# Kernel optimization log

Hardware: AMD Instinct MI355X
Metric: run time of the kernel (lower is better)

Reference implementation:

```python
import jax, jax.numpy as jnp
import numpy as np

E = 1024   # embedding_size
H = 16     # num_heads
DH = E // H


def setup_inputs() -> dict:
    key = jax.random.key(0)
    ks = jax.random.split(key, 11)
    B, S = 2, 2048
    std = 0.02
    return {
        "query": jax.random.normal(ks[0], (B, S, E), jnp.float32),
        "key": jax.random.normal(ks[1], (B, S, E), jnp.float32),
        "value": jax.random.normal(ks[2], (B, S, E), jnp.float32),
        "Wq": jax.random.normal(ks[3], (E, E), jnp.float32) * std,
        "bq": jnp.zeros((E,), jnp.float32),
        "Wk": jax.random.normal(ks[4], (E, E), jnp.float32) * std,
        "bk": jnp.zeros((E,), jnp.float32),
        "Wv": jax.random.normal(ks[5], (E, E), jnp.float32) * std,
        "bv": jnp.zeros((E,), jnp.float32),
        "Wo": jax.random.normal(ks[6], (E, E), jnp.float32) * std,
        "bo": jnp.zeros((E,), jnp.float32),
    }


def _split_heads(x, B, S):
    # [B,S,E] -> [B,H,S,DH]
    return x.reshape(B, S, H, DH).transpose(0, 2, 1, 3)


def reference(query, key, value, Wq, bq, Wk, bk, Wv, bv, Wo, bo):
    B, S, _ = query.shape
    # torch Linear: y = x @ W.T + b
    q = _split_heads(query @ Wq.T + bq, B, S)
    k = _split_heads(key @ Wk.T + bk, B, key.shape[1])
    v = _split_heads(value @ Wv.T + bv, B, value.shape[1])
    # naive unscaled attention (original has no 1/sqrt(d) factor)
    scores = jnp.einsum("bhsd,bhtd->bhst", q, k)  # [B,H,S,T]
    attn = jax.nn.softmax(scores, axis=-1)
    out = jnp.einsum("bhst,bhtd->bhsd", attn, v)  # [B,H,S,DH]
    out = out.transpose(0, 2, 1, 3).reshape(B, S, E)
    return out @ Wo.T + bo
```

## Files before the change

### kernel.cpp

```cpp
#include <hip/hip_runtime.h>
#include <hip/hip_bf16.h>

constexpr int kB   = 2;
constexpr int kS   = 2048;
constexpr int kE   = 1024;
constexpr int kH   = 16;
constexpr int kDH  = 64;
constexpr int kTok = kB * kS;

typedef short bf16x8 __attribute__((ext_vector_type(8)));
typedef float f32x4  __attribute__((ext_vector_type(4)));
typedef unsigned int uint2v __attribute__((ext_vector_type(2)));

__device__ __forceinline__ float bf2f(unsigned short s) {
  union { unsigned int u; float f; } c; c.u = ((unsigned int)s) << 16; return c.f;
}
__device__ __forceinline__ unsigned short f2bf(float f) {
  union { float f; unsigned int u; } c; c.f = f;
  unsigned int u = c.u;
  u += 0x7fffu + ((u >> 16) & 1u);
  return (unsigned short)(u >> 16);
}

__device__ __forceinline__ unsigned cvtpk(float lo, float hi) {
  unsigned r;
  asm("v_cvt_pk_bf16_f32 %0, %1, %2" : "=v"(r) : "v"(lo), "v"(hi));
  return r;
}

__device__ __forceinline__ void gl_lds16(const unsigned short* g, unsigned short* l) {
  __builtin_amdgcn_global_load_lds(
      (const __attribute__((address_space(1))) unsigned int*)g,
      (__attribute__((address_space(3))) unsigned int*)l, 16, 0, 0);
}

__global__ void detect_dtype(const unsigned short* __restrict__ q, int* flag) {
  __shared__ int cnt;
  if (threadIdx.x == 0) cnt = 0;
  __syncthreads();
  int bad = 0;
  for (int i = threadIdx.x; i < 4096; i += 256) {
    unsigned int e = (q[i] >> 7) & 0xFF;
    if (e >= 0xC0) bad++;
  }
  atomicAdd(&cnt, bad);
  __syncthreads();
  if (threadIdx.x == 0) *flag = (cnt > 8) ? 1 : 0;
}

struct Seg { const void* src; unsigned short* dst; unsigned int n; unsigned int blk0; };
struct ConvArgs { Seg s[11]; };

__global__ __launch_bounds__(256) void conv_all(ConvArgs a, const int* __restrict__ flag) {
  const unsigned int bid = blockIdx.x;
  int si = 0;
  #pragma unroll
  for (int i = 1; i < 11; ++i)
    if (bid >= a.s[i].blk0) si = i;
  const Seg sg = a.s[si];
  const int i0 = ((int)(bid - sg.blk0) * 256 + threadIdx.x) * 8;
  if (i0 >= (int)sg.n) return;
  if (*flag) {
    const float* s = (const float*)sg.src + i0;
    f32x4 f0 = *(const f32x4*)(s);
    f32x4 f1 = *(const f32x4*)(s + 4);
    bf16x8 v;
    #pragma unroll
    for (int j = 0; j < 4; ++j) v[j]     = (short)f2bf(f0[j]);
    #pragma unroll
    for (int j = 0; j < 4; ++j) v[j + 4] = (short)f2bf(f1[j]);
    *(bf16x8*)&sg.dst[i0] = v;
  } else {
    *(bf16x8*)&sg.dst[i0] = *(const bf16x8*)((const unsigned short*)sg.src + i0);
  }
}

__device__ __forceinline__ void gemm_core(
    const unsigned short* __restrict__ A,
    const unsigned short* __restrict__ W,
    int Kdim, int bM, int bN,
    unsigned short* As, unsigned short* Ws,
    f32x4 acc[4][4])
{
  const int tid  = threadIdx.x;
  const int lane = tid & 63;
  const int wv   = tid >> 6;
  const int wm   = (wv >> 1) * 64;
  const int wn   = (wv & 1) * 64;
  const int lr   = lane & 15;
  const int kq   = (lane >> 4) * 8;

  const int r0 = tid >> 2;
  const int c0 = (tid & 3) * 8;

  const unsigned short* Ag = A + (size_t)(bM + r0) * Kdim + c0;
  const unsigned short* Wg = W + (size_t)(bN + r0) * Kdim + c0;
  unsigned short* lA = &As[tid * 8];
  unsigned short* lW = &Ws[tid * 8];

  for (int k0 = 0; k0 < Kdim; k0 += 32) {
    gl_lds16(Ag + k0,                      lA);
    gl_lds16(Ag + (size_t)64 * Kdim + k0,  lA + 2048);
    gl_lds16(Wg + k0,                      lW);
    gl_lds16(Wg + (size_t)64 * Kdim + k0,  lW + 2048);
    __syncthreads();

    bf16x8 a[4], b[4];
    #pragma unroll
    for (int i = 0; i < 4; ++i)
      a[i] = *(const bf16x8*)&As[(wm + i * 16 + lr) * 32 + kq];
    #pragma unroll
    for (int i = 0; i < 4; ++i)
      b[i] = *(const bf16x8*)&Ws[(wn + i * 16 + lr) * 32 + kq];
    #pragma unroll
    for (int i = 0; i < 4; ++i)
      #pragma unroll
      for (int j = 0; j < 4; ++j)
        acc[i][j] = __builtin_amdgcn_mfma_f32_16x16x32_bf16(a[i], b[j], acc[i][j], 0, 0, 0);
    __syncthreads();
  }
}

__global__ __launch_bounds__(256) void gemm_qkv(
    const unsigned short* __restrict__ Abase,
    const unsigned short* __restrict__ Wbase,
    const unsigned short* __restrict__ biasbase,
    unsigned short* __restrict__ Cbase)
{
  __shared__ unsigned short As[128 * 32];
  __shared__ unsigned short Ws[128 * 32];

  const int z = blockIdx.z;
  const unsigned short* A    = Abase    + (size_t)z * (kTok * kE);
  const unsigned short* W    = Wbase    + (size_t)z * (kE * kE);
  const unsigned short* bias = biasbase + (size_t)z * kE;
  unsigned short* C          = Cbase    + (size_t)z * (kTok * kE);

  const int bM = blockIdx.y * 128;
  const int bN = blockIdx.x * 128;

  f32x4 acc[4][4] = {};
  gemm_core(A, W, kE, bM, bN, As, Ws, acc);

  const int lane = threadIdx.x & 63;
  const int wv   = threadIdx.x >> 6;
  const int wm   = (wv >> 1) * 64;
  const int wn   = (wv & 1) * 64;
  const int lr   = lane & 15;
  const int qd   = lane >> 4;
  #pragma unroll
  for (int j = 0; j < 4; ++j) {
    const int col = bN + wn + j * 16 + lr;
    const float bb = bf2f(bias[col]);
    #pragma unroll
    for (int i = 0; i < 4; ++i)
      #pragma unroll
      for (int r = 0; r < 4; ++r) {
        const int row = bM + wm + i * 16 + qd * 4 + r;
        C[(size_t)row * kE + col] = f2bf(acc[i][j][r] + bb);
      }
  }
}

__global__ __launch_bounds__(256) void vtrans(
    const unsigned short* __restrict__ Vb,
    unsigned short* __restrict__ Vt)
{
  __shared__ unsigned short Lt[64 * 72];
  const int tid = threadIdx.x;
  const int bh  = blockIdx.y;
  const int b   = bh >> 4;
  const int h   = bh & 15;
  const int hcol = h * kDH;
  const int s0  = blockIdx.x * 64;

  #pragma unroll
  for (int issue = 0; issue < 2; ++issue) {
    int g = issue * 256 + tid;
    int r = g >> 3, c = (g & 7) * 8;
    bf16x8 vv = *(const bf16x8*)&Vb[(size_t)(b * kS + s0 + r) * kE + hcol + c];
    const int swz = ((((r >> 3) ^ (c >> 3)) & 7) << 3) + (r & 7);
    #pragma unroll
    for (int i = 0; i < 8; ++i)
      Lt[(c + i) * 72 + swz] = (unsigned short)vv[i];
  }
  __syncthreads();
  #pragma unroll
  for (int issue = 0; issue < 2; ++issue) {
    int g = issue * 256 + tid;
    int f = g >> 3, tc = (g & 7) * 8;
    const int blk = ((tc >> 3) ^ (f >> 3)) & 7;
    bf16x8 vv = *(const bf16x8*)&Lt[f * 72 + (blk << 3)];
    *(bf16x8*)&Vt[(size_t)b * (kE * kS) + (size_t)(hcol + f) * kS + s0 + tc] = vv;
  }
}

__global__ __launch_bounds__(256) void gemm_out(
    const unsigned short* __restrict__ A,
    const unsigned short* __restrict__ W,
    const unsigned short* __restrict__ bias,
    void* __restrict__ C,
    const int* __restrict__ flag)
{
  __shared__ unsigned short As[128 * 32];
  __shared__ unsigned short Ws[128 * 32];

  const int bM = blockIdx.y * 128;
  const int bN = blockIdx.x * 128;

  f32x4 acc[4][4] = {};
  gemm_core(A, W, kE, bM, bN, As, Ws, acc);

  const int lane = threadIdx.x & 63;
  const int wv   = threadIdx.x >> 6;
  const int wm   = (wv >> 1) * 64;
  const int wn   = (wv & 1) * 64;
  const int lr   = lane & 15;
  const int qd   = lane >> 4;
  if (*flag) {
    float* Cf = (float*)C;
    #pragma unroll
    for (int j = 0; j < 4; ++j) {
      const int col = bN + wn + j * 16 + lr;
      const float bb = bf2f(bias[col]);
      #pragma unroll
      for (int i = 0; i < 4; ++i)
        #pragma unroll
        for (int r = 0; r < 4; ++r) {
          const int row = bM + wm + i * 16 + qd * 4 + r;
          Cf[(size_t)row * kE + col] = acc[i][j][r] + bb;
        }
    }
  } else {
    unsigned short* Cb = (unsigned short*)C;
    #pragma unroll
    for (int j = 0; j < 4; ++j) {
      const int col = bN + wn + j * 16 + lr;
      const float bb = bf2f(bias[col]);
      #pragma unroll
      for (int i = 0; i < 4; ++i)
        #pragma unroll
        for (int r = 0; r < 4; ++r) {
          const int row = bM + wm + i * 16 + qd * 4 + r;
          Cb[(size_t)row * kE + col] = f2bf(acc[i][j][r] + bb);
        }
    }
  }
}

__global__ __launch_bounds__(256) void attn(
    const unsigned short* __restrict__ Qb,
    const unsigned short* __restrict__ Kb,
    const unsigned short* __restrict__ Vt,
    unsigned short* __restrict__ Ob)
{
  __shared__ unsigned short Ks[64 * 72];
  __shared__ unsigned short Vs[64 * 72];

  const int tid  = threadIdx.x;
  const int lane = tid & 63;
  const int w    = tid >> 6;
  const int lr   = lane & 15;
  const int quad = lane >> 4;
  const int kq   = quad * 8;

  const int bh = blockIdx.y;
  const int b  = bh >> 4;
  const int h  = bh & 15;
  const int q0 = blockIdx.x * 128;

  const size_t rowbase = (size_t)b * kS * kE;
  const int hcol = h * kDH;
  const unsigned short* Vbase = Vt + (size_t)b * (kE * kS) + (size_t)hcol * kS;

  const int r0 = tid >> 3;
  const int c0 = (tid & 7) * 8;

  bf16x8 aq[2][2];
  #pragma unroll
  for (int rg = 0; rg < 2; ++rg)
    #pragma unroll
    for (int hh = 0; hh < 2; ++hh)
      aq[rg][hh] = *(const bf16x8*)
          &Qb[rowbase + (size_t)(q0 + w * 32 + rg * 16 + lr) * kE + hcol + hh * 32 + kq];

  f32x4 o[2][4] = {};
  float l4[2][4] = {};

  bf16x8 rk0 = *(const bf16x8*)&Kb[rowbase + (size_t)(r0)      * kE + hcol + c0];
  bf16x8 rk1 = *(const bf16x8*)&Kb[rowbase + (size_t)(r0 + 32) * kE + hcol + c0];
  bf16x8 rv0 = *(const bf16x8*)&Vbase[(size_t)(r0)      * kS + c0];
  bf16x8 rv1 = *(const bf16x8*)&Vbase[(size_t)(r0 + 32) * kS + c0];

  for (int t0 = 0; t0 < kS; t0 += 64) {
    __syncthreads();
    *(bf16x8*)&Ks[ r0       * 72 + c0] = rk0;
    *(bf16x8*)&Ks[(r0 + 32) * 72 + c0] = rk1;
    *(bf16x8*)&Vs[ r0       * 72 + c0] = rv0;
    *(bf16x8*)&Vs[(r0 + 32) * 72 + c0] = rv1;
    __syncthreads();

    const int t1 = t0 + 64;
    if (t1 < kS) {
      rk0 = *(const bf16x8*)&Kb[rowbase + (size_t)(t1 + r0)      * kE + hcol + c0];
      rk1 = *(const bf16x8*)&Kb[rowbase + (size_t)(t1 + r0 + 32) * kE + hcol + c0];
      rv0 = *(const bf16x8*)&Vbase[(size_t)(r0)      * kS + t1 + c0];
      rv1 = *(const bf16x8*)&Vbase[(size_t)(r0 + 32) * kS + t1 + c0];
    }

    f32x4 s[2][4];
    #pragma unroll
    for (int rg = 0; rg < 2; ++rg)
      #pragma unroll
      for (int tn = 0; tn < 4; ++tn)
        s[rg][tn] = f32x4{0.f, 0.f, 0.f, 0.f};
    #pragma unroll
    for (int tn = 0; tn < 4; ++tn) {
      const bf16x8 bk0 = *(const bf16x8*)&Ks[(tn * 16 + lr) * 72 + 0 + kq];
      const bf16x8 bk1 = *(const bf16x8*)&Ks[(tn * 16 + lr) * 72 + 32 + kq];
      #pragma unroll
      for (int rg = 0; rg < 2; ++rg) {
        s[rg][tn] = __builtin_amdgcn_mfma_f32_16x16x32_bf16(bk0, aq[rg][0], s[rg][tn], 0, 0, 0);
        s[rg][tn] = __builtin_amdgcn_mfma_f32_16x16x32_bf16(bk1, aq[rg][1], s[rg][tn], 0, 0, 0);
      }
    }

    #pragma unroll
    for (int rg = 0; rg < 2; ++rg)
      #pragma unroll
      for (int tn = 0; tn < 4; ++tn)
        #pragma unroll
        for (int r = 0; r < 4; ++r) {
          const float e = __expf(s[rg][tn][r]);
          s[rg][tn][r] = e;
          l4[rg][r] += e;
        }

    bf16x8 ap[2][2];
    #pragma unroll
    for (int rg = 0; rg < 2; ++rg)
      #pragma unroll
      for (int kk = 0; kk < 2; ++kk) {
        const unsigned A0 = cvtpk(s[rg][2 * kk][0],     s[rg][2 * kk][1]);
        const unsigned A1 = cvtpk(s[rg][2 * kk + 1][0], s[rg][2 * kk + 1][1]);
        const uint2v u   = __builtin_amdgcn_permlane32_swap(A0, A1, false, false);
        const uint2v z02 = __builtin_amdgcn_permlane16_swap(u[0], u[1], false, false);
        const unsigned B0 = cvtpk(s[rg][2 * kk][2],     s[rg][2 * kk][3]);
        const unsigned B1 = cvtpk(s[rg][2 * kk + 1][2], s[rg][2 * kk + 1][3]);
        const uint2v v2  = __builtin_amdgcn_permlane32_swap(B0, B1, false, false);
        const uint2v z13 = __builtin_amdgcn_permlane16_swap(v2[0], v2[1], false, false);
        union { unsigned ud[4]; bf16x8 v; } pk;
        pk.ud[0] = z02[0];
        pk.ud[1] = z13[0];
        pk.ud[2] = z02[1];
        pk.ud[3] = z13[1];
        ap[rg][kk] = pk.v;
      }

    #pragma unroll
    for (int kk = 0; kk < 2; ++kk)
      #pragma unroll
      for (int dt = 0; dt < 4; ++dt) {
        const bf16x8 bv = *(const bf16x8*)&Vs[(dt * 16 + lr) * 72 + kk * 32 + kq];
        #pragma unroll
        for (int rg = 0; rg < 2; ++rg)
          o[rg][dt] = __builtin_amdgcn_mfma_f32_16x16x32_bf16(ap[rg][kk], bv, o[rg][dt], 0, 0, 0);
      }
  }

  #pragma unroll
  for (int rg = 0; rg < 2; ++rg) {
    float l = (l4[rg][0] + l4[rg][1]) + (l4[rg][2] + l4[rg][3]);
    l += __shfl_xor(l, 16, 64);
    l += __shfl_xor(l, 32, 64);
    float inv[4];
    #pragma unroll
    for (int r = 0; r < 4; ++r)
      inv[r] = 1.0f / __shfl(l, quad * 4 + r, 64);

    #pragma unroll
    for (int dt = 0; dt < 4; ++dt) {
      #pragma unroll
      for (int r = 0; r < 4; ++r) {
        const int row = q0 + w * 32 + rg * 16 + quad * 4 + r;
        const int col = hcol + dt * 16 + lr;
        Ob[rowbase + (size_t)row * kE + col] = f2bf(o[rg][dt][r] * inv[r]);
      }
    }
  }
}

extern "C" void kernel_launch(void* const* d_in, const int* in_sizes, int n_in,
                              void* d_out, int out_size, void* d_ws, size_t ws_size,
                              hipStream_t stream) {
  const int nQKV = kTok * kE;
  const int nW   = kE * kE;
  const int nB   = kE;

  char* wsb = (char*)d_ws;
  int* flag = (int*)wsb;
  unsigned short* qc  = (unsigned short*)(wsb + 16);
  unsigned short* kc  = qc  + (size_t)nQKV;
  unsigned short* vc  = kc  + (size_t)nQKV;
  unsigned short* Wqc = vc  + (size_t)nQKV;
  unsigned short* Wkc = Wqc + (size_t)nW;
  unsigned short* Wvc = Wkc + (size_t)nW;
  unsigned short* Woc = Wvc + (size_t)nW;
  unsigned short* bqc = Woc + (size_t)nW;
  unsigned short* bkc = bqc + nB;
  unsigned short* bvc = bkc + nB;
  unsigned short* boc = bvc + nB;
  unsigned short* Qb  = boc + nB;
  unsigned short* Kb  = Qb  + (size_t)nQKV;
  unsigned short* Vb  = Kb  + (size_t)nQKV;
  unsigned short* Vtb = kc;
  unsigned short* Ob  = qc;

  detect_dtype<<<1, 256, 0, stream>>>((const unsigned short*)d_in[0], flag);

  ConvArgs ca;
  const void* srcs[11] = { d_in[0], d_in[1], d_in[2], d_in[3], d_in[4], d_in[5],
                           d_in[6], d_in[7], d_in[8], d_in[9], d_in[10] };
  unsigned short* dsts[11] = { qc, kc, vc, Wqc, bqc, Wkc, bkc, Wvc, bvc, Woc, boc };
  const unsigned int ns[11] = { (unsigned)nQKV, (unsigned)nQKV, (unsigned)nQKV,
                                (unsigned)nW, (unsigned)nB, (unsigned)nW, (unsigned)nB,
                                (unsigned)nW, (unsigned)nB, (unsigned)nW, (unsigned)nB };
  unsigned int blk = 0;
  for (int i = 0; i < 11; ++i) {
    ca.s[i].src = srcs[i]; ca.s[i].dst = dsts[i]; ca.s[i].n = ns[i]; ca.s[i].blk0 = blk;
    blk += (ns[i] + 2047) / 2048;
  }
  conv_all<<<blk, 256, 0, stream>>>(ca, flag);

  dim3 blk256(256);
  dim3 gqkv(kE / 128, kTok / 128, 3);
  gemm_qkv<<<gqkv, blk256, 0, stream>>>(qc, Wqc, bqc, Qb);

  dim3 gvt(kS / 64, kB * kH);
  vtrans<<<gvt, blk256, 0, stream>>>(Vb, Vtb);

  dim3 gattn(kS / 128, kB * kH);
  attn<<<gattn, blk256, 0, stream>>>(Qb, Kb, Vtb, Ob);

  dim3 gout(kE / 128, kTok / 128);
  gemm_out<<<gout, blk256, 0, stream>>>(Ob, Woc, boc, d_out, flag);
}
```

Baseline: 267.6 us.

## Double-buffer K/V tiles in attention and fold log2e into Wq for exp2

```diff
diff --git a/kernel.cpp b/kernel.cpp
--- a/kernel.cpp
+++ b/kernel.cpp
@@ -8,6 +8,8 @@
 constexpr int kDH  = 64;
 constexpr int kTok = kB * kS;
 
+constexpr float kLog2e = 1.4426950408889634f;
+
 typedef short bf16x8 __attribute__((ext_vector_type(8)));
 typedef float f32x4  __attribute__((ext_vector_type(4)));
 typedef unsigned int uint2v __attribute__((ext_vector_type(2)));
@@ -25,6 +27,12 @@
 __device__ __forceinline__ unsigned cvtpk(float lo, float hi) {
   unsigned r;
   asm("v_cvt_pk_bf16_f32 %0, %1, %2" : "=v"(r) : "v"(lo), "v"(hi));
+  return r;
+}
+
+__device__ __forceinline__ float fexp2(float x) {
+  float r;
+  asm("v_exp_f32 %0, %1" : "=v"(r) : "v"(x));
   return r;
 }
 
@@ -49,7 +57,7 @@
 }
 
 struct Seg { const void* src; unsigned short* dst; unsigned int n; unsigned int blk0; };
-struct ConvArgs { Seg s[11]; };
+struct ConvArgs { Seg s[11]; float scale[11]; };
 
 __global__ __launch_bounds__(256) void conv_all(ConvArgs a, const int* __restrict__ flag) {
   const unsigned int bid = blockIdx.x;
@@ -58,6 +66,7 @@
   for (int i = 1; i < 11; ++i)
     if (bid >= a.s[i].blk0) si = i;
   const Seg sg = a.s[si];
+  const float sc = a.scale[si];
   const int i0 = ((int)(bid - sg.blk0) * 256 + threadIdx.x) * 8;
   if (i0 >= (int)sg.n) return;
   if (*flag) {
@@ -66,12 +75,18 @@
     f32x4 f1 = *(const f32x4*)(s + 4);
     bf16x8 v;
     #pragma unroll
-    for (int j = 0; j < 4; ++j) v[j]     = (short)f2bf(f0[j]);
-    #pragma unroll
-    for (int j = 0; j < 4; ++j) v[j + 4] = (short)f2bf(f1[j]);
+    for (int j = 0; j < 4; ++j) v[j]     = (short)f2bf(f0[j] * sc);
+    #pragma unroll
+    for (int j = 0; j < 4; ++j) v[j + 4] = (short)f2bf(f1[j] * sc);
     *(bf16x8*)&sg.dst[i0] = v;
   } else {
-    *(bf16x8*)&sg.dst[i0] = *(const bf16x8*)((const unsigned short*)sg.src + i0);
+    bf16x8 v = *(const bf16x8*)((const unsigned short*)sg.src + i0);
+    if (sc != 1.0f) {
+      #pragma unroll
+      for (int j = 0; j < 8; ++j)
+        v[j] = (short)f2bf(bf2f((unsigned short)v[j]) * sc);
+    }
+    *(bf16x8*)&sg.dst[i0] = v;
   }
 }
 
@@ -254,8 +269,8 @@
     const unsigned short* __restrict__ Vt,
     unsigned short* __restrict__ Ob)
 {
-  __shared__ unsigned short Ks[64 * 72];
-  __shared__ unsigned short Vs[64 * 72];
+  __shared__ unsigned short Ks[2][64 * 72];
+  __shared__ unsigned short Vs[2][64 * 72];
 
   const int tid  = threadIdx.x;
   const int lane = tid & 63;
@@ -291,21 +306,32 @@
   bf16x8 rk1 = *(const bf16x8*)&Kb[rowbase + (size_t)(r0 + 32) * kE + hcol + c0];
   bf16x8 rv0 = *(const bf16x8*)&Vbase[(size_t)(r0)      * kS + c0];
   bf16x8 rv1 = *(const bf16x8*)&Vbase[(size_t)(r0 + 32) * kS + c0];
+  *(bf16x8*)&Ks[0][ r0       * 72 + c0] = rk0;
+  *(bf16x8*)&Ks[0][(r0 + 32) * 72 + c0] = rk1;
+  *(bf16x8*)&Vs[0][ r0       * 72 + c0] = rv0;
+  *(bf16x8*)&Vs[0][(r0 + 32) * 72 + c0] = rv1;
+  rk0 = *(const bf16x8*)&Kb[rowbase + (size_t)(64 + r0)      * kE + hcol + c0];
+  rk1 = *(const bf16x8*)&Kb[rowbase + (size_t)(64 + r0 + 32) * kE + hcol + c0];
+  rv0 = *(const bf16x8*)&Vbase[(size_t)(r0)      * kS + 64 + c0];
+  rv1 = *(const bf16x8*)&Vbase[(size_t)(r0 + 32) * kS + 64 + c0];
+  __syncthreads();
 
   for (int t0 = 0; t0 < kS; t0 += 64) {
-    __syncthreads();
-    *(bf16x8*)&Ks[ r0       * 72 + c0] = rk0;
-    *(bf16x8*)&Ks[(r0 + 32) * 72 + c0] = rk1;
-    *(bf16x8*)&Vs[ r0       * 72 + c0] = rv0;
-    *(bf16x8*)&Vs[(r0 + 32) * 72 + c0] = rv1;
-    __syncthreads();
-
-    const int t1 = t0 + 64;
-    if (t1 < kS) {
-      rk0 = *(const bf16x8*)&Kb[rowbase + (size_t)(t1 + r0)      * kE + hcol + c0];
-      rk1 = *(const bf16x8*)&Kb[rowbase + (size_t)(t1 + r0 + 32) * kE + hcol + c0];
-      rv0 = *(const bf16x8*)&Vbase[(size_t)(r0)      * kS + t1 + c0];
-      rv1 = *(const bf16x8*)&Vbase[(size_t)(r0 + 32) * kS + t1 + c0];
+    const int cur = (t0 >> 6) & 1;
+    const int nxt = cur ^ 1;
+
+    if (t0 + 64 < kS) {
+      *(bf16x8*)&Ks[nxt][ r0       * 72 + c0] = rk0;
+      *(bf16x8*)&Ks[nxt][(r0 + 32) * 72 + c0] = rk1;
+      *(bf16x8*)&Vs[nxt][ r0       * 72 + c0] = rv0;
+      *(bf16x8*)&Vs[nxt][(r0 + 32) * 72 + c0] = rv1;
+    }
+    if (t0 + 128 < kS) {
+      const int t2 = t0 + 128;
+      rk0 = *(const bf16x8*)&Kb[rowbase + (size_t)(t2 + r0)      * kE + hcol + c0];
+      rk1 = *(const bf16x8*)&Kb[rowbase + (size_t)(t2 + r0 + 32) * kE + hcol + c0];
+      rv0 = *(const bf16x8*)&Vbase[(size_t)(r0)      * kS + t2 + c0];
+      rv1 = *(const bf16x8*)&Vbase[(size_t)(r0 + 32) * kS + t2 + c0];
     }
 
     f32x4 s[2][4];
@@ -314,16 +340,18 @@
       #pragma unroll
       for (int tn = 0; tn < 4; ++tn)
         s[rg][tn] = f32x4{0.f, 0.f, 0.f, 0.f};
+    __builtin_amdgcn_s_setprio(1);
     #pragma unroll
     for (int tn = 0; tn < 4; ++tn) {
-      const bf16x8 bk0 = *(const bf16x8*)&Ks[(tn * 16 + lr) * 72 + 0 + kq];
-      const bf16x8 bk1 = *(const bf16x8*)&Ks[(tn * 16 + lr) * 72 + 32 + kq];
+      const bf16x8 bk0 = *(const bf16x8*)&Ks[cur][(tn * 16 + lr) * 72 + 0 + kq];
+      const bf16x8 bk1 = *(const bf16x8*)&Ks[cur][(tn * 16 + lr) * 72 + 32 + kq];
       #pragma unroll
       for (int rg = 0; rg < 2; ++rg) {
         s[rg][tn] = __builtin_amdgcn_mfma_f32_16x16x32_bf16(bk0, aq[rg][0], s[rg][tn], 0, 0, 0);
         s[rg][tn] = __builtin_amdgcn_mfma_f32_16x16x32_bf16(bk1, aq[rg][1], s[rg][tn], 0, 0, 0);
       }
     }
+    __builtin_amdgcn_s_setprio(0);
 
     #pragma unroll
     for (int rg = 0; rg < 2; ++rg)
@@ -331,7 +359,7 @@
       for (int tn = 0; tn < 4; ++tn)
         #pragma unroll
         for (int r = 0; r < 4; ++r) {
-          const float e = __expf(s[rg][tn][r]);
+          const float e = fexp2(s[rg][tn][r]);
           s[rg][tn][r] = e;
           l4[rg][r] += e;
         }
@@ -357,15 +385,19 @@
         ap[rg][kk] = pk.v;
       }
 
+    __builtin_amdgcn_s_setprio(1);
     #pragma unroll
     for (int kk = 0; kk < 2; ++kk)
       #pragma unroll
       for (int dt = 0; dt < 4; ++dt) {
-        const bf16x8 bv = *(const bf16x8*)&Vs[(dt * 16 + lr) * 72 + kk * 32 + kq];
+        const bf16x8 bv = *(const bf16x8*)&Vs[cur][(dt * 16 + lr) * 72 + kk * 32 + kq];
         #pragma unroll
         for (int rg = 0; rg < 2; ++rg)
           o[rg][dt] = __builtin_amdgcn_mfma_f32_16x16x32_bf16(ap[rg][kk], bv, o[rg][dt], 0, 0, 0);
       }
+    __builtin_amdgcn_s_setprio(0);
+
+    __syncthreads();
   }
 
   #pragma unroll
@@ -428,8 +460,11 @@
   unsigned int blk = 0;
   for (int i = 0; i < 11; ++i) {
     ca.s[i].src = srcs[i]; ca.s[i].dst = dsts[i]; ca.s[i].n = ns[i]; ca.s[i].blk0 = blk;
+    ca.scale[i] = 1.0f;
     blk += (ns[i] + 2047) / 2048;
   }
+  ca.scale[3] = kLog2e;
+  ca.scale[4] = kLog2e;
   conv_all<<<blk, 256, 0, stream>>>(ca, flag);
 
   dim3 blk256(256);
```

New measurement: 261.7 us. 2.2% less time.
